# Optimization experiments

Measured on AMD Instinct MI355X. Metric: run time of the kernel, lower is better.

Reference implementation:

```python
import jax, jax.numpy as jnp
import numpy as np

IMG = 512
C = 3
PS = 16
G = 32
B = 64
NH = IMG // PS
NW = IMG // PS
NP_ = NH * NW
P2 = PS * PS


def setup_inputs() -> dict:
    key = jax.random.key(0)
    k1, k2, k3, k4 = jax.random.split(key, 4)
    x = jax.random.normal(k1, (B, C, IMG, IMG), dtype=jnp.float32)
    # Conv2d(1, ps*ps, kernel=ps) default init ~ U(-1/ps, 1/ps); scale random normals similarly.
    obfuscation_weights = jax.random.normal(k2, (C, G, P2, P2), dtype=jnp.float32) / PS
    obfuscation_biases = jax.random.normal(k3, (C, G, P2), dtype=jnp.float32) / PS
    channel_permutation = jax.random.permutation(k4, jnp.arange(C, dtype=jnp.int32))
    return {
        "x": x,
        "obfuscation_weights": obfuscation_weights,
        "obfuscation_biases": obfuscation_biases,
        "channel_permutation": channel_permutation,
    }


def reference(x, obfuscation_weights, obfuscation_biases, channel_permutation):
    # x: (B, C, H, W) -> patches (B, C, N, ps*ps)
    x_patched = (
        x.reshape(B, C, NH, PS, NW, PS)
        .transpose(0, 1, 2, 4, 3, 5)
        .reshape(B, C, NP_, P2)
    )
    # group index per spatial patch: (row + col) % group_size
    ridx = jnp.arange(NH)[:, None]
    cidx = jnp.arange(NW)[None, :]
    group_map = ((ridx + cidx) % G).reshape(-1)  # (N,)
    sel_w = obfuscation_weights[:, group_map]  # (C, N, P2, P2)
    sel_b = obfuscation_biases[:, group_map]  # (C, N, P2)
    out = jnp.einsum("bcnp,cnpo->bcno", x_patched, sel_w) + sel_b
    # back to image layout
    out = (
        out.reshape(B, C, NH, NW, PS, PS)
        .transpose(0, 1, 2, 4, 3, 5)
        .reshape(B, C, IMG, IMG)
    )
    out = out[:, channel_permutation]
    return jnp.tanh(out)
```

## Files before the change

### kernel.cpp

```cpp
#include <hip/hip_runtime.h>

#define C_SZ   3
#define IMG_SZ 512

typedef short  short8 __attribute__((ext_vector_type(8)));
typedef float  f32x4  __attribute__((ext_vector_type(4)));
typedef unsigned short u16;
typedef u16    u16x8  __attribute__((ext_vector_type(8)));

__device__ __forceinline__ u16 f2bf(float f) {
    unsigned u = __float_as_uint(f);
    u += 0x7FFFu + ((u >> 16) & 1u);
    return (u16)(u >> 16);
}

__device__ __forceinline__ float tanh_fast(float v) {
    float e = __expf(2.f * v);
    return 1.f - 2.f * __builtin_amdgcn_rcpf(e + 1.f);
}

__device__ __forceinline__ void gload_lds16(const float* g, float* l) {
    __builtin_amdgcn_global_load_lds(
        (const __attribute__((address_space(1))) void*)g,
        (__attribute__((address_space(3))) void*)l, 16, 0, 0);
}

__device__ __forceinline__ short8 gload_b128(const u16* p) {
    short8 d;
    asm volatile("global_load_dwordx4 %0, %1, off"
                 : "=v"(d) : "v"(p) : "memory");
    return d;
}

__global__ __launch_bounds__(256)
void prep_wt(const float* __restrict__ w, u16* __restrict__ wt) {
    const int cg = blockIdx.x;
    const int kb = blockIdx.y;
    __shared__ float T[32][260];
    const int tid = threadIdx.x;
    const float* wb = w + (size_t)cg * 65536 + (size_t)kb * 32 * 256;
    #pragma unroll
    for (int pass = 0; pass < 8; ++pass) {
        int q = pass * 256 + tid;
        int pl = q >> 6, o4 = (q & 63) * 4;
        float4 v = *reinterpret_cast<const float4*>(wb + (size_t)pl * 256 + o4);
        T[pl][o4 + 0] = v.x; T[pl][o4 + 1] = v.y;
        T[pl][o4 + 2] = v.z; T[pl][o4 + 3] = v.w;
    }
    __syncthreads();
    u16* dst = wt + ((size_t)cg * 8 + kb) * 8192;
    #pragma unroll
    for (int h0 = 0; h0 < 4; ++h0) {
        int h = h0 * 256 + tid;
        int kg = h >> 8, n = h & 255;
        u16x8 v;
        #pragma unroll
        for (int e = 0; e < 8; ++e) v[e] = f2bf(T[kg * 8 + e][n]);
        *reinterpret_cast<u16x8*>(dst + (size_t)kg * 2048 + n * 8) = v;
    }
}

__global__ __launch_bounds__(256)
void obf_mfma(const float* __restrict__ x,
              const u16*  __restrict__ wt,
              const float* __restrict__ bias,
              const int*  __restrict__ perm,
              float* __restrict__ out)
{
    const int bid  = blockIdx.x;
    const int sbid = (bid & 7) * 384 + (bid >> 3);
    const int mtile = sbid & 31;
    const int cg    = sbid >> 5;
    const int c = cg >> 5, g = cg & 31;
    const int tid  = threadIdx.x;
    const int lane = tid & 63, wv = tid >> 6;
    const int r = lane & 15, kg = lane >> 4;

    __shared__ float As[3][2048];

    int cp = 0;
    #pragma unroll
    for (int i = 0; i < C_SZ; ++i) if (perm[i] == c) cp = i;

    const float* g_src[2];
    #pragma unroll
    for (int j = 0; j < 2; ++j) {
        int q    = wv * 128 + j * 64 + lane;
        int row  = q >> 3;
        int lpos = (q & 7) ^ (row & 7);
        int mg   = mtile * 64 + row;
        int b    = mg >> 5, nh = mg & 31, nw = (g - nh) & 31;
        g_src[j] = x + (((size_t)(b * C_SZ + c) * IMG_SZ + nh * 16 + (lpos >> 2)) * IMG_SZ
                        + nw * 16 + (lpos & 3) * 4);
    }
    const u16* bsrc = wt + (size_t)cg * 65536 + kg * 2048 + (size_t)(wv * 64 + r) * 8;

    const int p0 = (((2 * kg)     ^ (r & 7)) * 4);
    const int p1 = (((2 * kg + 1) ^ (r & 7)) * 4);
    const int rbase = r * 32;

    f32x4 acc[4][4] = {};
    short8 bv[2][4];

#define STAGE_A(t) do {                                                \
        float* d_ = &As[(t) % 3][0] + wv * 512;                        \
        gload_lds16(g_src[0] + (size_t)(t) * 1024, d_);                \
        gload_lds16(g_src[1] + (size_t)(t) * 1024, d_ + 256);          \
    } while (0)

    STAGE_A(0);
    #pragma unroll
    for (int ni = 0; ni < 4; ++ni)
        bv[0][ni] = gload_b128(bsrc + ni * 128);

    #pragma unroll
    for (int t = 0; t < 8; ++t) {
        if (t < 7) {
            STAGE_A(t + 1);
            #pragma unroll
            for (int ni = 0; ni < 4; ++ni)
                bv[(t + 1) & 1][ni] = gload_b128(bsrc + (t + 1) * 8192 + ni * 128);
            asm volatile("s_waitcnt vmcnt(6)" ::: "memory");
        } else {
            asm volatile("s_waitcnt vmcnt(0)" ::: "memory");
        }
        __builtin_amdgcn_sched_barrier(0);
        __builtin_amdgcn_s_barrier();

        const float* lb = &As[t % 3][0];
        #pragma unroll
        for (int mi = 0; mi < 4; ++mi) {
            f32x4 v0 = *reinterpret_cast<const f32x4*>(lb + mi * 512 + rbase + p0);
            f32x4 v1 = *reinterpret_cast<const f32x4*>(lb + mi * 512 + rbase + p1);
            short8 af;
            af[0] = (short)f2bf(v0[0]); af[1] = (short)f2bf(v0[1]);
            af[2] = (short)f2bf(v0[2]); af[3] = (short)f2bf(v0[3]);
            af[4] = (short)f2bf(v1[0]); af[5] = (short)f2bf(v1[1]);
            af[6] = (short)f2bf(v1[2]); af[7] = (short)f2bf(v1[3]);
            #pragma unroll
            for (int ni = 0; ni < 4; ++ni)
                acc[mi][ni] = __builtin_amdgcn_mfma_f32_16x16x32_bf16(
                    af, bv[t & 1][ni], acc[mi][ni], 0, 0, 0);
        }
    }
#undef STAGE_A

    const int cc = lane & 15;
    float bs[4];
    #pragma unroll
    for (int ni = 0; ni < 4; ++ni)
        bs[ni] = bias[(size_t)cg * 256 + wv * 64 + ni * 16 + cc];

    #pragma unroll
    for (int mi = 0; mi < 4; ++mi) {
        #pragma unroll
        for (int reg = 0; reg < 4; ++reg) {
            const int ml = mi * 16 + kg * 4 + reg;
            const int mg = mtile * 64 + ml;
            const int b  = mg >> 5, nh = mg & 31, nw = (g - nh) & 31;
            float* orow = out + ((size_t)(b * C_SZ + cp) * IMG_SZ + nh * 16) * IMG_SZ
                              + nw * 16 + cc;
            #pragma unroll
            for (int ni = 0; ni < 4; ++ni) {
                const int rp = wv * 4 + ni;
                orow[(size_t)rp * IMG_SZ] = tanh_fast(acc[mi][ni][reg] + bs[ni]);
            }
        }
    }
}

extern "C" void kernel_launch(void* const* d_in, const int* in_sizes, int n_in,
                              void* d_out, int out_size, void* d_ws, size_t ws_size,
                              hipStream_t stream) {
    const float* x    = (const float*)d_in[0];
    const float* w    = (const float*)d_in[1];
    const float* bias = (const float*)d_in[2];
    const int*   perm = (const int*)d_in[3];
    float* out = (float*)d_out;
    u16*   wt  = (u16*)d_ws;

    dim3 pgrid(C_SZ * 32, 8, 1);
    prep_wt<<<pgrid, 256, 0, stream>>>(w, wt);

    obf_mfma<<<3072, 256, 0, stream>>>(x, wt, bias, perm, out);
}
```

Before: 145.7 us.

## Halve M-tile per block to 32 rows, raise occupancy, drop B double buffering

Each block now covers 32 patch rows instead of 64, so the grid doubles to 6144 blocks and LDS per block halves. Accumulators drop from 4x4 to 2x4, launch bounds request 5 blocks per CU, and B fragments are loaded each iteration without double buffering. The fp32-to-bf16 packing now uses the paired HIP intrinsic. The aim is more resident waves to hide memory latency. The cost is that each block reads the weight tile twice as often relative to its output, and B loads are no longer prefetched one step ahead.

```diff
diff --git a/kernel.cpp b/kernel.cpp
--- a/kernel.cpp
+++ b/kernel.cpp
@@ -1,4 +1,5 @@
 #include <hip/hip_runtime.h>
+#include <hip/hip_bf16.h>
 
 #define C_SZ   3
 #define IMG_SZ 512
@@ -12,6 +13,12 @@
     unsigned u = __float_as_uint(f);
     u += 0x7FFFu + ((u >> 16) & 1u);
     return (u16)(u >> 16);
+}
+
+__device__ __forceinline__ unsigned pkbf(float lo, float hi) {
+    union { __hip_bfloat162 h; unsigned u; } cv;
+    cv.h = __float22bfloat162_rn(make_float2(lo, hi));
+    return cv.u;
 }
 
 __device__ __forceinline__ float tanh_fast(float v) {
@@ -60,7 +67,7 @@
     }
 }
 
-__global__ __launch_bounds__(256)
+__global__ __launch_bounds__(256, 5)
 void obf_mfma(const float* __restrict__ x,
               const u16*  __restrict__ wt,
               const float* __restrict__ bias,
@@ -68,59 +75,49 @@
               float* __restrict__ out)
 {
     const int bid  = blockIdx.x;
-    const int sbid = (bid & 7) * 384 + (bid >> 3);
-    const int mtile = sbid & 31;
-    const int cg    = sbid >> 5;
+    const int sbid = (bid & 7) * 768 + (bid >> 3);
+    const int mtile = sbid & 63;
+    const int cg    = sbid >> 6;
     const int c = cg >> 5, g = cg & 31;
     const int tid  = threadIdx.x;
     const int lane = tid & 63, wv = tid >> 6;
     const int r = lane & 15, kg = lane >> 4;
 
-    __shared__ float As[3][2048];
+    __shared__ float As[3][1024];
 
     int cp = 0;
     #pragma unroll
     for (int i = 0; i < C_SZ; ++i) if (perm[i] == c) cp = i;
 
-    const float* g_src[2];
-    #pragma unroll
-    for (int j = 0; j < 2; ++j) {
-        int q    = wv * 128 + j * 64 + lane;
-        int row  = q >> 3;
-        int lpos = (q & 7) ^ (row & 7);
-        int mg   = mtile * 64 + row;
-        int b    = mg >> 5, nh = mg & 31, nw = (g - nh) & 31;
-        g_src[j] = x + (((size_t)(b * C_SZ + c) * IMG_SZ + nh * 16 + (lpos >> 2)) * IMG_SZ
-                        + nw * 16 + (lpos & 3) * 4);
+    const float* g_src;
+    {
+        int lr   = wv * 8 + (lane >> 3);
+        int lch  = (lane & 7) ^ (lr & 7);
+        int R    = mtile * 32 + lr;
+        int b    = R >> 5, nh = R & 31, nw = (g - nh) & 31;
+        g_src = x + (((size_t)(b * C_SZ + c) * IMG_SZ + nh * 16 + (lch >> 2)) * IMG_SZ
+                     + nw * 16 + (lch & 3) * 4);
     }
     const u16* bsrc = wt + (size_t)cg * 65536 + kg * 2048 + (size_t)(wv * 64 + r) * 8;
 
-    const int p0 = (((2 * kg)     ^ (r & 7)) * 4);
-    const int p1 = (((2 * kg + 1) ^ (r & 7)) * 4);
-    const int rbase = r * 32;
+    f32x4 acc[2][4] = {};
+    short8 bv[4];
 
-    f32x4 acc[4][4] = {};
-    short8 bv[2][4];
-
-#define STAGE_A(t) do {                                                \
-        float* d_ = &As[(t) % 3][0] + wv * 512;                        \
-        gload_lds16(g_src[0] + (size_t)(t) * 1024, d_);                \
-        gload_lds16(g_src[1] + (size_t)(t) * 1024, d_ + 256);          \
+#define STAGE_A(t) do {                                                   \
+        float* d_ = &As[(t) % 3][0] + wv * 256;                           \
+        gload_lds16(g_src + (size_t)(t) * 1024, d_);                      \
     } while (0)
 
     STAGE_A(0);
-    #pragma unroll
-    for (int ni = 0; ni < 4; ++ni)
-        bv[0][ni] = gload_b128(bsrc + ni * 128);
 
     #pragma unroll
     for (int t = 0; t < 8; ++t) {
+        #pragma unroll
+        for (int ni = 0; ni < 4; ++ni)
+            bv[ni] = gload_b128(bsrc + (size_t)t * 8192 + ni * 128);
         if (t < 7) {
             STAGE_A(t + 1);
-            #pragma unroll
-            for (int ni = 0; ni < 4; ++ni)
-                bv[(t + 1) & 1][ni] = gload_b128(bsrc + (t + 1) * 8192 + ni * 128);
-            asm volatile("s_waitcnt vmcnt(6)" ::: "memory");
+            asm volatile("s_waitcnt vmcnt(1)" ::: "memory");
         } else {
             asm volatile("s_waitcnt vmcnt(0)" ::: "memory");
         }
@@ -129,34 +126,37 @@
 
         const float* lb = &As[t % 3][0];
         #pragma unroll
-        for (int mi = 0; mi < 4; ++mi) {
-            f32x4 v0 = *reinterpret_cast<const f32x4*>(lb + mi * 512 + rbase + p0);
-            f32x4 v1 = *reinterpret_cast<const f32x4*>(lb + mi * 512 + rbase + p1);
-            short8 af;
-            af[0] = (short)f2bf(v0[0]); af[1] = (short)f2bf(v0[1]);
-            af[2] = (short)f2bf(v0[2]); af[3] = (short)f2bf(v0[3]);
-            af[4] = (short)f2bf(v1[0]); af[5] = (short)f2bf(v1[1]);
-            af[6] = (short)f2bf(v1[2]); af[7] = (short)f2bf(v1[3]);
+        for (int mi = 0; mi < 2; ++mi) {
+            const int rowoff = (mi * 16 + r) * 32;
+            f32x4 v0 = *reinterpret_cast<const f32x4*>(
+                lb + rowoff + (((2 * kg)     ^ (r & 7)) * 4));
+            f32x4 v1 = *reinterpret_cast<const f32x4*>(
+                lb + rowoff + (((2 * kg + 1) ^ (r & 7)) * 4));
+            union { short8 s; uint4 u; } A_;
+            A_.u.x = pkbf(v0[0], v0[1]);
+            A_.u.y = pkbf(v0[2], v0[3]);
+            A_.u.z = pkbf(v1[0], v1[1]);
+            A_.u.w = pkbf(v1[2], v1[3]);
             #pragma unroll
             for (int ni = 0; ni < 4; ++ni)
                 acc[mi][ni] = __builtin_amdgcn_mfma_f32_16x16x32_bf16(
-                    af, bv[t & 1][ni], acc[mi][ni], 0, 0, 0);
+                    A_.s, bv[ni], acc[mi][ni], 0, 0, 0);
         }
     }
 #undef STAGE_A
 
-    const int cc = lane & 15;
+    const int cc = r;
     float bs[4];
     #pragma unroll
     for (int ni = 0; ni < 4; ++ni)
         bs[ni] = bias[(size_t)cg * 256 + wv * 64 + ni * 16 + cc];
 
     #pragma unroll
-    for (int mi = 0; mi < 4; ++mi) {
+    for (int mi = 0; mi < 2; ++mi) {
         #pragma unroll
         for (int reg = 0; reg < 4; ++reg) {
             const int ml = mi * 16 + kg * 4 + reg;
-            const int mg = mtile * 64 + ml;
+            const int mg = mtile * 32 + ml;
             const int b  = mg >> 5, nh = mg & 31, nw = (g - nh) & 31;
             float* orow = out + ((size_t)(b * C_SZ + cp) * IMG_SZ + nh * 16) * IMG_SZ
                               + nw * 16 + cc;
@@ -182,5 +182,5 @@
     dim3 pgrid(C_SZ * 32, 8, 1);
     prep_wt<<<pgrid, 256, 0, stream>>>(w, wt);
 
-    obf_mfma<<<3072, 256, 0, stream>>>(x, wt, bias, perm, out);
+    obf_mfma<<<6144, 256, 0, stream>>>(x, wt, bias, perm, out);
 }
```

Result: slower. 177.0 us (+21.5%).
